# Optimization experiments

Measured on AMD Instinct MI355X. Metric: run time of the kernel, lower is better.

The kernel has to match this reference:

```python
import jax, jax.numpy as jnp
import numpy as np

NUM_HEADS = 16
KEY_DIM = 64
VALUE_DIM = 64
D_MODEL = 1024
NEG_INF = -1e10


def setup_inputs() -> dict:
    key = jax.random.key(0)
    ks = jax.random.split(key, 8)
    B, T, S, D = 4, 2048, 2048, D_MODEL
    w_scale = 1.0 / np.sqrt(D)  # keep logits well-scaled
    inp = {
        'query': jax.random.normal(ks[0], (B, T, D), jnp.float32),
        'key':   jax.random.normal(ks[1], (B, S, D), jnp.float32),
        'value': jax.random.normal(ks[2], (B, S, D), jnp.float32),
        'Wq': jax.random.normal(ks[3], (D, NUM_HEADS * KEY_DIM), jnp.float32) * w_scale,
        'bq': jnp.zeros((NUM_HEADS * KEY_DIM,), jnp.float32),
        'Wk': jax.random.normal(ks[4], (D, NUM_HEADS * KEY_DIM), jnp.float32) * w_scale,
        'bk': jnp.zeros((NUM_HEADS * KEY_DIM,), jnp.float32),
        'Wv': jax.random.normal(ks[5], (D, NUM_HEADS * VALUE_DIM), jnp.float32) * w_scale,
        'bv': jnp.zeros((NUM_HEADS * VALUE_DIM,), jnp.float32),
        'Wo': jax.random.normal(ks[6], (NUM_HEADS * VALUE_DIM, D), jnp.float32) * w_scale,
        'bo': jnp.zeros((D,), jnp.float32),
    }
    return inp


def reference(query, key, value, Wq, bq, Wk, bk, Wv, bv, Wo, bo):
    B, T, _ = query.shape
    S = key.shape[1]
    H, Dk, Dv = NUM_HEADS, KEY_DIM, VALUE_DIM
    # QKV projections -> (B, T/S, H, D_head)
    q = (query @ Wq + bq).reshape(B, T, H, Dk)
    k = (key @ Wk + bk).reshape(B, S, H, Dk)
    v = (value @ Wv + bv).reshape(B, S, H, Dv)
    # scaled dot-product scores: (B, H, T, S)
    q = q * (1.0 / jnp.sqrt(jnp.asarray(Dk, q.dtype)))
    scores = jnp.einsum('bthd,bshd->bhts', q, k)
    # causal mask [1,1,T,S], additive -1e10 on masked positions (as in source)
    causal = jnp.tril(jnp.ones((T, S), scores.dtype))
    scores = scores + NEG_INF * (1.0 - causal)
    attn = jax.nn.softmax(scores, axis=-1)
    # dropout rate = 0.0 -> identity
    ctx = jnp.einsum('bhts,bshd->bthd', attn, v).reshape(B, T, H * Dv)
    out = ctx @ Wo + bo
    return out
```

## Files before the change

### kernel.cpp

```cpp
#include <hip/hip_runtime.h>
#include <cstdint>

#define DEV static __device__ __forceinline__

typedef unsigned short u16;
typedef unsigned int u32;
using short8 = __attribute__((ext_vector_type(8))) short;
using f32x2  = __attribute__((ext_vector_type(2))) float;
using f32x4  = __attribute__((ext_vector_type(4))) float;
using f32x8  = __attribute__((ext_vector_type(8))) float;
using f32x16 = __attribute__((ext_vector_type(16))) float;
using u32x4  = __attribute__((ext_vector_type(4))) unsigned int;

constexpr int Bz = 4, Tz = 2048, Dz = 1024, Hz = 16;
constexpr float QSCALE = 0.125f * 1.4426950408889634f;

DEV u16 f2bf(float x) {
  union { float f; u32 u; } c; c.f = x;
  u32 u = c.u;
  return (u16)((u + 0x7FFFu + ((u >> 16) & 1u)) >> 16);
}

DEV u32 cvtpk(float a, float b) {
  u32 r;
  asm("v_cvt_pk_bf16_f32 %0, %1, %2" : "=v"(r) : "v"(a), "v"(b));
  return r;
}

DEV void gload16(const void* g, void* l) {
  __builtin_amdgcn_global_load_lds(
      (const __attribute__((address_space(1))) void*)g,
      (__attribute__((address_space(3))) void*)l, 16, 0, 0);
}

__global__ __launch_bounds__(256) void cvt_kernel(
    const float* __restrict__ Xq, const float* __restrict__ Xk,
    const float* __restrict__ Xv, u16* __restrict__ Yq,
    u16* __restrict__ Yk, u16* __restrict__ Yv) {
  int z = blockIdx.y;
  const float* X = z == 0 ? Xq : z == 1 ? Xk : Xv;
  u16* Y         = z == 0 ? Yq : z == 1 ? Yk : Yv;
  size_t i = (size_t)blockIdx.x * 256 + threadIdx.x;
  float4 a = ((const float4*)X)[i * 2];
  float4 b = ((const float4*)X)[i * 2 + 1];
  uint4 o;
  o.x = cvtpk(a.x, a.y); o.y = cvtpk(a.z, a.w);
  o.z = cvtpk(b.x, b.y); o.w = cvtpk(b.z, b.w);
  ((uint4*)Y)[i] = o;
}

__global__ void wt_kernel(const float* __restrict__ W0, const float* __restrict__ W1,
                          const float* __restrict__ W2, const float* __restrict__ W3,
                          u16* __restrict__ T0, u16* __restrict__ T1,
                          u16* __restrict__ T2, u16* __restrict__ T3) {
  __shared__ float tile[32][33];
  int z = blockIdx.z;
  const float* W = z == 0 ? W0 : z == 1 ? W1 : z == 2 ? W2 : W3;
  u16* WT = z == 0 ? T0 : z == 1 ? T1 : z == 2 ? T2 : T3;
  int n0 = blockIdx.x * 32, k0 = blockIdx.y * 32;
  int tx = threadIdx.x & 31, ty = threadIdx.x >> 5;
  #pragma unroll
  for (int i = 0; i < 32; i += 8)
    tile[ty + i][tx] = W[(size_t)(k0 + ty + i) * Dz + n0 + tx];
  __syncthreads();
  #pragma unroll
  for (int i = 0; i < 32; i += 8)
    WT[(size_t)(n0 + ty + i) * Dz + k0 + tx] = f2bf(tile[tx][ty + i]);
}

__global__ __launch_bounds__(256) void vt_kernel(const u16* __restrict__ V,
                                                 u16* __restrict__ VT) {
  __shared__ char t[8192];
  int bh = blockIdx.y, tt0 = blockIdx.x * 64;
  int b = bh >> 4, h = bh & 15;
  int tid = threadIdx.x;
  const char* src = (const char*)(V + ((size_t)(b * Tz + tt0)) * Dz + h * 64);
  #pragma unroll
  for (int i = 0; i < 2; ++i) {
    int c = tid + i * 256;
    int row = c >> 3, colb = (c & 7) * 16;
    *(uint4*)(t + row * 128 + (colb ^ ((row & 7) << 4))) =
        *(const uint4*)(src + (size_t)row * (Dz * 2) + colb);
  }
  __syncthreads();
  int dv = tid >> 2, ts = (tid & 3) * 16;
  u32 w[8];
  #pragma unroll
  for (int p = 0; p < 8; ++p) {
    int t1 = ts + 2 * p, t2 = t1 + 1;
    u32 lo = *(const u16*)(t + t1 * 128 + ((dv * 2) ^ ((t1 & 7) << 4)));
    u32 hi = *(const u16*)(t + t2 * 128 + ((dv * 2) ^ ((t2 & 7) << 4)));
    w[p] = lo | (hi << 16);
  }
  u16* dst = VT + ((size_t)bh * 64 + dv) * Tz + tt0 + ts;
  *(uint4*)(dst)     = uint4{w[0], w[1], w[2], w[3]};
  *(uint4*)(dst + 8) = uint4{w[4], w[5], w[6], w[7]};
}

template <int EPI>
DEV void gemm_core(const u16* __restrict__ A, const u16* __restrict__ WT,
                   const float* __restrict__ bias, void* __restrict__ Cptr,
                   float scale, int n0, int m0, char* L)
{
  const int tid = threadIdx.x;
  const int lane = tid & 63, wid = tid >> 6;
  const int g = lane >> 4, l15 = lane & 15;
  const int wm = (wid >> 1) * 64, wn = (wid & 1) * 64;

  f32x4 acc[4][4] = {};

  const int srow = tid >> 3, scolb = (tid & 7) * 16;
  const int scbs = scolb ^ ((srow & 7) << 4);

  for (int step = 0; step < 16; ++step) {
    const int k0 = step * 64;
    #pragma unroll
    for (int i = 0; i < 4; ++i) {
      int row = srow + i * 32;
      gload16(A + (size_t)(m0 + row) * Dz + k0 + (scbs >> 1),
              L + (tid + i * 256) * 16);
    }
    #pragma unroll
    for (int i = 0; i < 4; ++i) {
      int row = srow + i * 32;
      gload16(WT + (size_t)(n0 + row) * Dz + k0 + (scbs >> 1),
              L + 16384 + (tid + i * 256) * 16);
    }
    __syncthreads();

    #pragma unroll
    for (int kc = 0; kc < 2; ++kc) {
      short8 af[4], bfv[4];
      #pragma unroll
      for (int mt = 0; mt < 4; ++mt) {
        int row = wm + mt * 16 + l15;
        af[mt] = *(const short8*)(L + row * 128 + ((kc * 64 + g * 16) ^ ((row & 7) << 4)));
      }
      #pragma unroll
      for (int nt = 0; nt < 4; ++nt) {
        int row = wn + nt * 16 + l15;
        bfv[nt] = *(const short8*)(L + 16384 + row * 128 + ((kc * 64 + g * 16) ^ ((row & 7) << 4)));
      }
      #pragma unroll
      for (int mt = 0; mt < 4; ++mt)
        #pragma unroll
        for (int nt = 0; nt < 4; ++nt)
          acc[mt][nt] = __builtin_amdgcn_mfma_f32_16x16x32_bf16(af[mt], bfv[nt], acc[mt][nt], 0, 0, 0);
    }
    __syncthreads();
  }

  if (EPI == 0) {
    u16* C = (u16*)Cptr;
    #pragma unroll
    for (int nt = 0; nt < 4; ++nt) {
      int n = n0 + wn + nt * 16 + l15;
      float bv = bias[n];
      #pragma unroll
      for (int mt = 0; mt < 4; ++mt)
        #pragma unroll
        for (int r = 0; r < 4; ++r) {
          int m = m0 + wm + mt * 16 + g * 4 + r;
          C[(size_t)m * Dz + n] = f2bf((acc[mt][nt][r] + bv) * scale);
        }
    }
  } else {
    float* C = (float*)Cptr;
    #pragma unroll
    for (int nt = 0; nt < 4; ++nt) {
      int n = n0 + wn + nt * 16 + l15;
      float bv = bias[n];
      #pragma unroll
      for (int mt = 0; mt < 4; ++mt)
        #pragma unroll
        for (int r = 0; r < 4; ++r) {
          int m = m0 + wm + mt * 16 + g * 4 + r;
          C[(size_t)m * Dz + n] = acc[mt][nt][r] + bv;
        }
    }
  }
}

__global__ __launch_bounds__(256, 4) void qkv_kernel(
    const u16* __restrict__ Aq, const u16* __restrict__ Ak, const u16* __restrict__ Av,
    const u16* __restrict__ Wq, const u16* __restrict__ Wk, const u16* __restrict__ Wv,
    const float* __restrict__ bq, const float* __restrict__ bk, const float* __restrict__ bv,
    u16* __restrict__ oq, u16* __restrict__ ok, u16* __restrict__ ov)
{
  __shared__ char lds[32768];
  int z = blockIdx.z;
  const u16* A   = z == 0 ? Aq : z == 1 ? Ak : Av;
  const u16* W   = z == 0 ? Wq : z == 1 ? Wk : Wv;
  const float* b = z == 0 ? bq : z == 1 ? bk : bv;
  u16* C         = z == 0 ? oq : z == 1 ? ok : ov;
  float scale    = z == 0 ? QSCALE : 1.0f;
  gemm_core<0>(A, W, b, C, scale, blockIdx.y * 128, blockIdx.x * 128, lds);
}

__global__ __launch_bounds__(256, 4) void out_gemm_kernel(
    const u16* __restrict__ A, const u16* __restrict__ WT,
    const float* __restrict__ bias, float* __restrict__ C)
{
  __shared__ char lds[32768];
  gemm_core<1>(A, WT, bias, C, 1.0f, blockIdx.y * 128, blockIdx.x * 128, lds);
}

DEV short8 mk_pb(float p0, float p1, float p2, float p3,
                 float p4, float p5, float p6, float p7) {
  u32 x0 = cvtpk(p0, p1), y0 = cvtpk(p4, p5);
  u32 x1 = cvtpk(p2, p3), y1 = cvtpk(p6, p7);
  asm("v_permlane32_swap_b32 %0, %1" : "+v"(x0), "+v"(y0));
  asm("v_permlane32_swap_b32 %0, %1" : "+v"(x1), "+v"(y1));
  u32x4 w = {x0, x1, y0, y1};
  return __builtin_bit_cast(short8, w);
}

DEV float vmax16(f32x16 a, f32x16 b) {
  f32x16 m = __builtin_elementwise_max(a, b);
  f32x8 m8 = __builtin_elementwise_max(
      __builtin_shufflevector(m, m, 0, 1, 2, 3, 4, 5, 6, 7),
      __builtin_shufflevector(m, m, 8, 9, 10, 11, 12, 13, 14, 15));
  f32x4 m4 = __builtin_elementwise_max(
      __builtin_shufflevector(m8, m8, 0, 1, 2, 3),
      __builtin_shufflevector(m8, m8, 4, 5, 6, 7));
  f32x2 m2 = __builtin_elementwise_max(
      __builtin_shufflevector(m4, m4, 0, 1),
      __builtin_shufflevector(m4, m4, 2, 3));
  return fmaxf(m2[0], m2[1]);
}
DEV float vsum16(f32x16 a, f32x16 b) {
  f32x16 s = a + b;
  f32x8 s8 = __builtin_shufflevector(s, s, 0, 1, 2, 3, 4, 5, 6, 7) +
             __builtin_shufflevector(s, s, 8, 9, 10, 11, 12, 13, 14, 15);
  f32x4 s4 = __builtin_shufflevector(s8, s8, 0, 1, 2, 3) +
             __builtin_shufflevector(s8, s8, 4, 5, 6, 7);
  f32x2 s2 = __builtin_shufflevector(s4, s4, 0, 1) +
             __builtin_shufflevector(s4, s4, 2, 3);
  return s2[0] + s2[1];
}

__global__ __launch_bounds__(512) void attn_kernel(
    const u16* __restrict__ Q, const u16* __restrict__ K,
    const u16* __restrict__ VT, u16* __restrict__ CTX)
{
  __shared__ char lds[65536];

  const int tid = threadIdx.x;
  const int lane = tid & 63, wave = tid >> 6;
  const int s = wave >> 2, w4 = wave & 3;
  const int l31 = lane & 31, hi = lane >> 5;
  const int pr = blockIdx.y;
  const int bh = blockIdx.x;
  const int b = bh >> 4, h = bh & 15;

  const u16* qb  = Q  + (size_t)b * Tz * Dz + h * 64;
  const u16* kb  = K  + (size_t)b * Tz * Dz + h * 64;
  const u16* vtb = VT + (size_t)bh * 64 * Tz;

  #pragma unroll 1
  for (int half = 0; half < 2; ++half) {
    const int j = half ? (15 - pr) : pr;
    const int t0 = j * 128;
    const int nsteps = j + 1;
    const int wq0 = t0 + w4 * 32;
    const int qg = wq0 + l31, wqhi = wq0 + 31;
    const int tbase = s * nsteps;

    auto stage = [&](int buf, int step) {
      #pragma unroll
      for (int i = 0; i < 4; ++i) {
        int c = tid + i * 512;
        int sc = c >> 10, r = c & 1023;
        int tn = r >> 9, e = r & 511;
        int row = e >> 3, colb = (e & 7) * 16;
        int cbs = colb ^ ((row & 7) << 4);
        int kv0 = (sc * nsteps + step) * 64;
        char* dst = lds + ((sc * 2 + buf) << 14) + (tn << 13) + e * 16;
        if (tn == 0)
          gload16(kb + (size_t)(kv0 + row) * Dz + (cbs >> 1), dst);
        else
          gload16(vtb + (size_t)row * Tz + kv0 + (cbs >> 1), dst);
      }
    };

    stage(0, 0);

    short8 qf[4];
    #pragma unroll
    for (int kc = 0; kc < 4; ++kc)
      qf[kc] = *(const short8*)(qb + (size_t)qg * Dz + kc * 16 + hi * 8);

    f32x16 o0 = {}, o1 = {};
    float m_run = -3.0e38f, l_run = 0.f;

    __syncthreads();

    int cur = 0;
    for (int step = 0; step < nsteps; ++step) {
      if (step + 1 < nsteps) stage(cur ^ 1, step + 1);
      const int kv0 = (tbase + step) * 64;

      if (kv0 <= wqhi) {
        const char* Kl = lds + ((s * 2 + cur) << 14);
        const char* Vl = Kl + 8192;
        const int swz = (l31 & 7) << 4;

        f32x16 s0 = {}, s1 = {};
        __builtin_amdgcn_s_setprio(1);
        #pragma unroll
        for (int kc = 0; kc < 4; ++kc) {
          int cb = (kc * 32 + hi * 16) ^ swz;
          short8 kf0 = *(const short8*)(Kl + l31 * 128 + cb);
          short8 kf1 = *(const short8*)(Kl + (32 + l31) * 128 + cb);
          s0 = __builtin_amdgcn_mfma_f32_32x32x16_bf16(kf0, qf[kc], s0, 0, 0, 0);
          s1 = __builtin_amdgcn_mfma_f32_32x32x16_bf16(kf1, qf[kc], s1, 0, 0, 0);
        }
        __builtin_amdgcn_s_setprio(0);

        if (kv0 + 63 > wq0) {
          #pragma unroll
          for (int r = 0; r < 16; ++r) {
            int kg = kv0 + (r & 3) + 8 * (r >> 2) + 4 * hi;
            if (kg > qg)      s0[r] = -3.0e38f;
            if (kg + 32 > qg) s1[r] = -3.0e38f;
          }
        }

        float tmax = vmax16(s0, s1);
        tmax = fmaxf(tmax, __shfl_xor(tmax, 32));

        if (__any(tmax > m_run + 8.f)) {
          float m_new = fmaxf(m_run, tmax);
          float sc = __builtin_amdgcn_exp2f(m_run - m_new);
          l_run *= sc;
          #pragma unroll
          for (int r = 0; r < 16; ++r) { o0[r] *= sc; o1[r] *= sc; }
          m_run = m_new;
        }
        #pragma unroll
        for (int r = 0; r < 16; ++r) {
          s0[r] = __builtin_amdgcn_exp2f(s0[r] - m_run);
          s1[r] = __builtin_amdgcn_exp2f(s1[r] - m_run);
        }
        float psum = vsum16(s0, s1);
        psum += __shfl_xor(psum, 32);
        l_run += psum;

        short8 pb0 = mk_pb(s0[0], s0[1], s0[2],  s0[3],  s0[4],  s0[5],  s0[6],  s0[7]);
        short8 pb1 = mk_pb(s0[8], s0[9], s0[10], s0[11], s0[12], s0[13], s0[14], s0[15]);
        short8 pb2 = mk_pb(s1[0], s1[1], s1[2],  s1[3],  s1[4],  s1[5],  s1[6],  s1[7]);
        short8 pb3 = mk_pb(s1[8], s1[9], s1[10], s1[11], s1[12], s1[13], s1[14], s1[15]);

        __builtin_amdgcn_s_setprio(1);
        #pragma unroll
        for (int kc = 0; kc < 4; ++kc) {
          int cb = (kc * 32 + hi * 16) ^ swz;
          short8 vf0 = *(const short8*)(Vl + l31 * 128 + cb);
          short8 vf1 = *(const short8*)(Vl + (32 + l31) * 128 + cb);
          short8 pbk = (kc == 0) ? pb0 : (kc == 1) ? pb1 : (kc == 2) ? pb2 : pb3;
          o0 = __builtin_amdgcn_mfma_f32_32x32x16_bf16(vf0, pbk, o0, 0, 0, 0);
          o1 = __builtin_amdgcn_mfma_f32_32x32x16_bf16(vf1, pbk, o1, 0, 0, 0);
        }
        __builtin_amdgcn_s_setprio(0);
      }

      __syncthreads();
      cur ^= 1;
    }

    if (s == 1) {
      char* P = lds + w4 * 9216 + lane * 144;
      #pragma unroll
      for (int r2 = 0; r2 < 4; ++r2) {
        f32x4 a = {o0[4*r2], o0[4*r2+1], o0[4*r2+2], o0[4*r2+3]};
        *(f32x4*)(P + r2 * 16) = a;
        f32x4 c = {o1[4*r2], o1[4*r2+1], o1[4*r2+2], o1[4*r2+3]};
        *(f32x4*)(P + 64 + r2 * 16) = c;
      }
      *(float*)(P + 128) = m_run;
      *(float*)(P + 132) = l_run;
    }
    __syncthreads();
    if (s == 0) {
      const char* P = lds + w4 * 9216 + lane * 144;
      float m1 = *(const float*)(P + 128), l1 = *(const float*)(P + 132);
      float m = fmaxf(m_run, m1);
      float w0 = __builtin_amdgcn_exp2f(m_run - m);
      float w1 = __builtin_amdgcn_exp2f(m1 - m);
      float inv = 1.0f / (w0 * l_run + w1 * l1);

      u16* cp = CTX + ((size_t)(b * Tz + qg)) * Dz + h * 64;
      #pragma unroll
      for (int rq = 0; rq < 4; ++rq) {
        f32x4 p0 = *(const f32x4*)(P + rq * 16);
        f32x4 p1 = *(const f32x4*)(P + 64 + rq * 16);
        int dv0 = 8 * rq + 4 * hi;
        float a0 = (w0 * o0[rq*4+0] + w1 * p0[0]) * inv;
        float a1 = (w0 * o0[rq*4+1] + w1 * p0[1]) * inv;
        float a2 = (w0 * o0[rq*4+2] + w1 * p0[2]) * inv;
        float a3 = (w0 * o0[rq*4+3] + w1 * p0[3]) * inv;
        *(uint2*)(cp + dv0) = make_uint2(cvtpk(a0, a1), cvtpk(a2, a3));
        float c0 = (w0 * o1[rq*4+0] + w1 * p1[0]) * inv;
        float c1 = (w0 * o1[rq*4+1] + w1 * p1[1]) * inv;
        float c2 = (w0 * o1[rq*4+2] + w1 * p1[2]) * inv;
        float c3 = (w0 * o1[rq*4+3] + w1 * p1[3]) * inv;
        *(uint2*)(cp + 32 + dv0) = make_uint2(cvtpk(c0, c1), cvtpk(c2, c3));
      }
    }
    __syncthreads();
  }
}

extern "C" void kernel_launch(void* const* d_in, const int* in_sizes, int n_in,
                              void* d_out, int out_size, void* d_ws, size_t ws_size,
                              hipStream_t stream) {
  (void)in_sizes; (void)n_in; (void)out_size; (void)ws_size;
  const float* query = (const float*)d_in[0];
  const float* key   = (const float*)d_in[1];
  const float* value = (const float*)d_in[2];
  const float* Wq = (const float*)d_in[3];
  const float* bq = (const float*)d_in[4];
  const float* Wk = (const float*)d_in[5];
  const float* bk = (const float*)d_in[6];
  const float* Wv = (const float*)d_in[7];
  const float* bv = (const float*)d_in[8];
  const float* Wo = (const float*)d_in[9];
  const float* bo = (const float*)d_in[10];

  char* ws = (char*)d_ws;
  const size_t SZ_ACT = (size_t)Bz * Tz * Dz * sizeof(u16);
  const size_t SZ_W = (size_t)Dz * Dz * sizeof(u16);
  u16* qw  = (u16*)(ws);
  u16* kw  = (u16*)(ws + SZ_ACT);
  u16* vw  = (u16*)(ws + 2 * SZ_ACT);
  u16* vtw = (u16*)(ws + 3 * SZ_ACT);
  u16* qx  = vtw;
  u16* cw  = vw;
  u16* wqt = (u16*)(ws + 4 * SZ_ACT);
  u16* wkt = (u16*)(ws + 4 * SZ_ACT + SZ_W);
  u16* wvt = (u16*)(ws + 4 * SZ_ACT + 2 * SZ_W);
  u16* wot = (u16*)(ws + 4 * SZ_ACT + 3 * SZ_W);
  u16* kx = (u16*)d_out;
  u16* vx = (u16*)d_out + (size_t)Bz * Tz * Dz;

  const int CVTG = (Bz * Tz * Dz) / (256 * 8);
  cvt_kernel<<<dim3(CVTG, 3), 256, 0, stream>>>(query, key, value, qx, kx, vx);

  wt_kernel<<<dim3(32, 32, 4), 256, 0, stream>>>(Wq, Wk, Wv, Wo, wqt, wkt, wvt, wot);

  qkv_kernel<<<dim3(64, 8, 3), 256, 0, stream>>>(qx, kx, vx,
                                                 wqt, wkt, wvt,
                                                 bq, bk, bv,
                                                 qw, kw, vw);

  vt_kernel<<<dim3(Tz / 64, Bz * Hz), 256, 0, stream>>>(vw, vtw);

  attn_kernel<<<dim3(Bz * Hz, 8), 512, 0, stream>>>(qw, kw, vtw, cw);

  out_gemm_kernel<<<dim3(64, 8), 256, 0, stream>>>(cw, wot, bo, (float*)d_out);
}
```

Before: 187.2 us.

## Fuse V transpose into QKV GEMM epilogue and single-buffer attention LDS

Removes the separate vt_kernel. The V projection's GEMM epilogue now writes its tile transposed through swizzled LDS straight into the per-head VT layout, which saves one launch and a full read and write of V. The attention kernel also drops K/V double buffering: LDS shrinks from 64KB to 36KB and each step does a synchronous stage followed by a barrier. This may raise occupancy but gives up the overlap of loads with compute.

```diff
diff --git a/kernel.cpp b/kernel.cpp
--- a/kernel.cpp
+++ b/kernel.cpp
@@ -68,35 +68,6 @@
     WT[(size_t)(n0 + ty + i) * Dz + k0 + tx] = f2bf(tile[tx][ty + i]);
 }
 
-__global__ __launch_bounds__(256) void vt_kernel(const u16* __restrict__ V,
-                                                 u16* __restrict__ VT) {
-  __shared__ char t[8192];
-  int bh = blockIdx.y, tt0 = blockIdx.x * 64;
-  int b = bh >> 4, h = bh & 15;
-  int tid = threadIdx.x;
-  const char* src = (const char*)(V + ((size_t)(b * Tz + tt0)) * Dz + h * 64);
-  #pragma unroll
-  for (int i = 0; i < 2; ++i) {
-    int c = tid + i * 256;
-    int row = c >> 3, colb = (c & 7) * 16;
-    *(uint4*)(t + row * 128 + (colb ^ ((row & 7) << 4))) =
-        *(const uint4*)(src + (size_t)row * (Dz * 2) + colb);
-  }
-  __syncthreads();
-  int dv = tid >> 2, ts = (tid & 3) * 16;
-  u32 w[8];
-  #pragma unroll
-  for (int p = 0; p < 8; ++p) {
-    int t1 = ts + 2 * p, t2 = t1 + 1;
-    u32 lo = *(const u16*)(t + t1 * 128 + ((dv * 2) ^ ((t1 & 7) << 4)));
-    u32 hi = *(const u16*)(t + t2 * 128 + ((dv * 2) ^ ((t2 & 7) << 4)));
-    w[p] = lo | (hi << 16);
-  }
-  u16* dst = VT + ((size_t)bh * 64 + dv) * Tz + tt0 + ts;
-  *(uint4*)(dst)     = uint4{w[0], w[1], w[2], w[3]};
-  *(uint4*)(dst + 8) = uint4{w[4], w[5], w[6], w[7]};
-}
-
 template <int EPI>
 DEV void gemm_core(const u16* __restrict__ A, const u16* __restrict__ WT,
                    const float* __restrict__ bias, void* __restrict__ Cptr,
@@ -164,7 +135,7 @@
           C[(size_t)m * Dz + n] = f2bf((acc[mt][nt][r] + bv) * scale);
         }
     }
-  } else {
+  } else if (EPI == 1) {
     float* C = (float*)Cptr;
     #pragma unroll
     for (int nt = 0; nt < 4; ++nt) {
@@ -177,6 +148,34 @@
           int m = m0 + wm + mt * 16 + g * 4 + r;
           C[(size_t)m * Dz + n] = acc[mt][nt][r] + bv;
         }
+    }
+  } else {
+    u16* VT = (u16*)Cptr;
+    #pragma unroll
+    for (int nt = 0; nt < 4; ++nt) {
+      int nrel = wn + nt * 16 + l15;
+      float bv = bias[n0 + nrel];
+      int swz = (nrel & 7) << 4;
+      #pragma unroll
+      for (int mt = 0; mt < 4; ++mt) {
+        int mrel0 = wm + mt * 16 + g * 4;
+        uint2 p = make_uint2(cvtpk(acc[mt][nt][0] + bv, acc[mt][nt][1] + bv),
+                             cvtpk(acc[mt][nt][2] + bv, acc[mt][nt][3] + bv));
+        *(uint2*)(L + nrel * 256 + ((mrel0 * 2) ^ swz)) = p;
+      }
+    }
+    __syncthreads();
+    int n = tid & 127, strip = tid >> 7;
+    int nn = n0 + n;
+    int h = nn >> 6, dv = nn & 63;
+    int b = m0 >> 11;
+    int tb = m0 & 2047;
+    int swz = (n & 7) << 4;
+    u16* dst = VT + (((size_t)(b * Hz + h) * 64 + dv) * Tz) + tb + strip * 64;
+    #pragma unroll
+    for (int c = 0; c < 8; ++c) {
+      uint4 v = *(const uint4*)(L + n * 256 + ((strip * 128 + c * 16) ^ swz));
+      *(uint4*)(dst + c * 8) = v;
     }
   }
 }
@@ -185,16 +184,17 @@
     const u16* __restrict__ Aq, const u16* __restrict__ Ak, const u16* __restrict__ Av,
     const u16* __restrict__ Wq, const u16* __restrict__ Wk, const u16* __restrict__ Wv,
     const float* __restrict__ bq, const float* __restrict__ bk, const float* __restrict__ bv,
-    u16* __restrict__ oq, u16* __restrict__ ok, u16* __restrict__ ov)
+    u16* __restrict__ oq, u16* __restrict__ ok, u16* __restrict__ ovt)
 {
   __shared__ char lds[32768];
   int z = blockIdx.z;
-  const u16* A   = z == 0 ? Aq : z == 1 ? Ak : Av;
-  const u16* W   = z == 0 ? Wq : z == 1 ? Wk : Wv;
-  const float* b = z == 0 ? bq : z == 1 ? bk : bv;
-  u16* C         = z == 0 ? oq : z == 1 ? ok : ov;
-  float scale    = z == 0 ? QSCALE : 1.0f;
-  gemm_core<0>(A, W, b, C, scale, blockIdx.y * 128, blockIdx.x * 128, lds);
+  int n0 = blockIdx.y * 128, m0 = blockIdx.x * 128;
+  if (z == 0)
+    gemm_core<0>(Aq, Wq, bq, oq, QSCALE, n0, m0, lds);
+  else if (z == 1)
+    gemm_core<0>(Ak, Wk, bk, ok, 1.0f, n0, m0, lds);
+  else
+    gemm_core<2>(Av, Wv, bv, ovt, 1.0f, n0, m0, lds);
 }
 
 __global__ __launch_bounds__(256, 4) void out_gemm_kernel(
@@ -243,7 +243,7 @@
     const u16* __restrict__ Q, const u16* __restrict__ K,
     const u16* __restrict__ VT, u16* __restrict__ CTX)
 {
-  __shared__ char lds[65536];
+  __shared__ char lds[36864];
 
   const int tid = threadIdx.x;
   const int lane = tid & 63, wave = tid >> 6;
@@ -266,7 +266,7 @@
     const int qg = wq0 + l31, wqhi = wq0 + 31;
     const int tbase = s * nsteps;
 
-    auto stage = [&](int buf, int step) {
+    auto stage = [&](int step) {
       #pragma unroll
       for (int i = 0; i < 4; ++i) {
         int c = tid + i * 512;
@@ -275,7 +275,7 @@
         int row = e >> 3, colb = (e & 7) * 16;
         int cbs = colb ^ ((row & 7) << 4);
         int kv0 = (sc * nsteps + step) * 64;
-        char* dst = lds + ((sc * 2 + buf) << 14) + (tn << 13) + e * 16;
+        char* dst = lds + (sc << 14) + (tn << 13) + e * 16;
         if (tn == 0)
           gload16(kb + (size_t)(kv0 + row) * Dz + (cbs >> 1), dst);
         else
@@ -283,8 +283,6 @@
       }
     };
 
-    stage(0, 0);
-
     short8 qf[4];
     #pragma unroll
     for (int kc = 0; kc < 4; ++kc)
@@ -293,15 +291,13 @@
     f32x16 o0 = {}, o1 = {};
     float m_run = -3.0e38f, l_run = 0.f;
 
-    __syncthreads();
-
-    int cur = 0;
     for (int step = 0; step < nsteps; ++step) {
-      if (step + 1 < nsteps) stage(cur ^ 1, step + 1);
+      stage(step);
+      __syncthreads();
       const int kv0 = (tbase + step) * 64;
 
       if (kv0 <= wqhi) {
-        const char* Kl = lds + ((s * 2 + cur) << 14);
+        const char* Kl = lds + (s << 14);
         const char* Vl = Kl + 8192;
         const int swz = (l31 & 7) << 4;
 
@@ -365,7 +361,6 @@
       }
 
       __syncthreads();
-      cur ^= 1;
     }
 
     if (s == 1) {
@@ -434,7 +429,7 @@
   u16* kw  = (u16*)(ws + SZ_ACT);
   u16* vw  = (u16*)(ws + 2 * SZ_ACT);
   u16* vtw = (u16*)(ws + 3 * SZ_ACT);
-  u16* qx  = vtw;
+  u16* qx  = vw;
   u16* cw  = vw;
   u16* wqt = (u16*)(ws + 4 * SZ_ACT);
   u16* wkt = (u16*)(ws + 4 * SZ_ACT + SZ_W);
@@ -451,9 +446,7 @@
   qkv_kernel<<<dim3(64, 8, 3), 256, 0, stream>>>(qx, kx, vx,
                                                  wqt, wkt, wvt,
                                                  bq, bk, bv,
-                                                 qw, kw, vw);
-
-  vt_kernel<<<dim3(Tz / 64, Bz * Hz), 256, 0, stream>>>(vw, vtw);
+                                                 qw, kw, vtw);
 
   attn_kernel<<<dim3(Bz * Hz, 8), 512, 0, stream>>>(qw, kw, vtw, cw);
 
```

Result: no change. 187.1 us (-0.1%).
